# Optimization experiments

Hardware: AMD Instinct MI355X
Metric: run time of the kernel (lower is better)

Reference implementation:

```python
import jax, jax.numpy as jnp
import numpy as np

HEADS = 8
HEAD_DIM = 32
DIM = 256        # embed_dim; inner_dim = HEADS*HEAD_DIM = 256
DEPTH = 2
MLP_DIM = 1024
GRID_H, GRID_W = 64, 64
CELL_DIM = 15    # pe(0) + in(3) + out(3) + hidden(9)
PE_IN = 3        # cell_pe_patch_dim + cell_in_patch_dim
UPDATE_DIM = 12  # cell_out(3) + hidden(9)
BATCH = 8


def layer_norm(x, g, b, eps=1e-5):
    m = jnp.mean(x, axis=-1, keepdims=True)
    v = jnp.var(x, axis=-1, keepdims=True)
    return (x - m) * jax.lax.rsqrt(v + eps) * g + b


def vit_positional_encoding(n, dim):
    pos = jnp.arange(n, dtype=jnp.float32)[:, None]
    div = jnp.exp(jnp.arange(0, dim, 2, dtype=jnp.float32) * (-np.log(10000.0) / dim))
    pe = jnp.zeros((n, dim), dtype=jnp.float32)
    pe = pe.at[:, 0::2].set(jnp.sin(pos * div)).at[:, 1::2].set(jnp.cos(pos * div))
    return pe[None]  # [1, n, dim]


def localize(x, H, W):
    # x: [b, heads, n, d] with n = H*W. Gather circular 3x3 neighbourhood per position
    # (equivalent to circular pad + one-hot conv in the torch LocalizeAttention).
    b, nh, n, d = x.shape
    y = x.reshape(b, nh, H, W, d)
    neigh = [jnp.roll(y, (1 - ki, 1 - kj), axis=(2, 3)) for ki in range(3) for kj in range(3)]
    return jnp.stack(neigh, axis=4).reshape(b, nh, n, 9, d)  # [b, h, n, 9, d]


def setup_inputs() -> dict:
    key = jax.random.key(0)
    ks = jax.random.split(key, 20)
    d = {}
    d['cells'] = jax.random.normal(ks[0], (BATCH, CELL_DIM, GRID_H, GRID_W), dtype=jnp.float32)
    s = 0.02
    d['We'] = jax.random.normal(ks[1], (CELL_DIM, DIM), jnp.float32) * s
    d['be'] = jnp.zeros((DIM,), jnp.float32)
    d['ln1_g'] = jnp.ones((DEPTH, DIM), jnp.float32)
    d['ln1_b'] = jnp.zeros((DEPTH, DIM), jnp.float32)
    d['Wqkv'] = jax.random.normal(ks[2], (DEPTH, DIM, 3 * HEADS * HEAD_DIM), jnp.float32) * s
    d['Wo'] = jax.random.normal(ks[3], (DEPTH, HEADS * HEAD_DIM, DIM), jnp.float32) * s
    d['bo'] = jnp.zeros((DEPTH, DIM), jnp.float32)
    d['ln2_g'] = jnp.ones((DEPTH, DIM), jnp.float32)
    d['ln2_b'] = jnp.zeros((DEPTH, DIM), jnp.float32)
    d['W1'] = jax.random.normal(ks[4], (DEPTH, DIM, MLP_DIM), jnp.float32) * s
    d['b1'] = jnp.zeros((DEPTH, MLP_DIM), jnp.float32)
    d['W2'] = jax.random.normal(ks[5], (DEPTH, MLP_DIM, DIM), jnp.float32) * s
    d['b2'] = jnp.zeros((DEPTH, DIM), jnp.float32)
    d['lnh_g'] = jnp.ones((DIM,), jnp.float32)
    d['lnh_b'] = jnp.zeros((DIM,), jnp.float32)
    # NOTE: torch zero-inits mlp_head; we use small random weights so the output is nontrivial.
    d['Wh'] = jax.random.normal(ks[6], (DIM, UPDATE_DIM), jnp.float32) * s
    d['bh'] = jnp.zeros((UPDATE_DIM,), jnp.float32)
    return d


def reference(cells, We, be, ln1_g, ln1_b, Wqkv, Wo, bo, ln2_g, ln2_b,
              W1, b1, W2, b2, lnh_g, lnh_b, Wh, bh):
    b, c, H, W = cells.shape
    n = H * W
    x = cells.reshape(b, c, n).transpose(0, 2, 1)           # b n c
    x = x @ We + be                                         # cell_to_embedding
    x = x + vit_positional_encoding(n, x.shape[-1])
    scale = HEAD_DIM ** -0.5
    for l in range(DEPTH):
        y = layer_norm(x, ln1_g[l], ln1_b[l])
        qkv = y @ Wqkv[l]                                   # b n 3*inner
        q, k, v = jnp.split(qkv, 3, axis=-1)
        split_heads = lambda t: t.reshape(b, n, HEADS, HEAD_DIM).transpose(0, 2, 1, 3)
        q, k, v = split_heads(q), split_heads(k), split_heads(v)  # b h n d
        kl = localize(k, H, W)                              # b h n 9 d
        vl = localize(v, H, W)
        dots = jnp.einsum('bhnd,bhnkd->bhnk', q, kl) * scale
        attn = jax.nn.softmax(dots, axis=-1)
        out = jnp.einsum('bhnk,bhnkd->bhnd', attn, vl)
        out = out.transpose(0, 2, 1, 3).reshape(b, n, HEADS * HEAD_DIM)
        x = out @ Wo[l] + bo[l] + x                         # attention + residual
        y = layer_norm(x, ln2_g[l], ln2_b[l])
        y = jax.nn.gelu(y @ W1[l] + b1[l], approximate=False) @ W2[l] + b2[l]
        x = x + y                                           # ffn + residual
    upd = layer_norm(x, lnh_g, lnh_b) @ Wh + bh             # b n UPDATE_DIM
    upd = upd.transpose(0, 2, 1).reshape(b, UPDATE_DIM, H, W)
    # update_rate = 1.0 -> deterministic branch: cells[:, PE_IN:] + update
    updated = cells[:, PE_IN:] + upd
    return jnp.concatenate([cells[:, :PE_IN], updated], axis=1)
```

## Files before the change

### kernel.cpp

```cpp
#include <hip/hip_runtime.h>
#include <hip/hip_bf16.h>
#include <math.h>

#define HEADS 8
#define HEAD_DIM 32
#define DIM 256
#define MLP_DIM 1024
#define NTOK 4096
#define BATCH 8
#define M_TOK (BATCH*NTOK)
#define CELL_DIM 15
#define PE_IN 3
#define UPD 12
#define HME ((size_t)M_TOK*32)

typedef __attribute__((ext_vector_type(8))) short bf16x8;
typedef __attribute__((ext_vector_type(4))) float f32x4;

static __device__ __forceinline__ float bf2f(unsigned short u) {
    return __uint_as_float(((unsigned int)u) << 16);
}
static __device__ __forceinline__ unsigned short f2bf(float f) {
    __hip_bfloat16 h = __float2bfloat16(f);
    union { __hip_bfloat16 h; unsigned short u; } cv; cv.h = h; return cv.u;
}
static __device__ __forceinline__ void gload_lds16(const unsigned short* g, unsigned short* l) {
    __builtin_amdgcn_global_load_lds(
        (const __attribute__((address_space(1))) void*)g,
        (__attribute__((address_space(3))) void*)l, 16, 0, 0);
}
static __device__ __forceinline__ float gelu_fast(float v) {
    return v / (1.f + __expf(-1.59576912f * (v + 0.044715f * v * v * v)));
}

__global__ __launch_bounds__(256) void k_embed(const float* __restrict__ cells,
        const float* __restrict__ We, const float* __restrict__ be,
        const float* __restrict__ g, const float* __restrict__ bln,
        unsigned short* __restrict__ x, unsigned short* __restrict__ y) {
    __shared__ float red[8];
    int tok = blockIdx.x;
    int d = threadIdx.x;
    int b = tok >> 12, n = tok & 4095;
    const float* cb = cells + (size_t)b * CELL_DIM * NTOK + n;
    float acc = 0.f;
#pragma unroll
    for (int c = 0; c < CELL_DIM; ++c)
        acc += cb[c * NTOK] * We[c * DIM + d];
    int i = d >> 1;
    float freq = __expf(-0.03597789f * (float)(2 * i));
    float ph = (float)n * freq;
    float pe = (d & 1) ? __cosf(ph) : __sinf(ph);
    float v = acc + be[d] + pe;
    x[(size_t)tok * DIM + d] = f2bf(v);
    float s = v, ss = v * v;
#pragma unroll
    for (int off = 32; off; off >>= 1) { s += __shfl_xor(s, off); ss += __shfl_xor(ss, off); }
    int wave = d >> 6, lane = d & 63;
    if (lane == 0) { red[wave] = s; red[4 + wave] = ss; }
    __syncthreads();
    float stot = red[0] + red[1] + red[2] + red[3];
    float sstot = red[4] + red[5] + red[6] + red[7];
    float mean = stot * (1.f / DIM);
    float rstd = rsqrtf(sstot * (1.f / DIM) - mean * mean + 1e-5f);
    y[(size_t)tok * DIM + d] = f2bf((v - mean) * rstd * g[d] + bln[d]);
}

__global__ __launch_bounds__(256) void k_prep(const float* __restrict__ Wqkv,
        const float* __restrict__ Wo, const float* __restrict__ W1,
        const float* __restrict__ W2, const float* __restrict__ Wh,
        unsigned short* __restrict__ wT) {
    int seg = blockIdx.y;
    int idx = blockIdx.x * 256 + threadIdx.x;
    if (seg == 8) {
        if (idx >= 16 * 256) return;
        int u = idx >> 8, k = idx & 255;
        wT[1572864 + idx] = (u < UPD) ? f2bf(Wh[(size_t)k * UPD + u]) : (unsigned short)0;
        return;
    }
    int l = seg >> 2, mat = seg & 3;
    const float* src; int kwSh, Nw; size_t ooff;
    switch (mat) {
        case 0: src = Wqkv + (size_t)l * 196608; kwSh = 8;  Nw = 768;  ooff = (size_t)l * 786432 + 0;      break;
        case 1: src = Wo   + (size_t)l * 65536;  kwSh = 8;  Nw = 256;  ooff = (size_t)l * 786432 + 196608; break;
        case 2: src = W1   + (size_t)l * 262144; kwSh = 8;  Nw = 1024; ooff = (size_t)l * 786432 + 262144; break;
        default:src = W2   + (size_t)l * 262144; kwSh = 10; Nw = 256;  ooff = (size_t)l * 786432 + 524288; break;
    }
    int Kw = 1 << kwSh;
    if (idx >= Kw * Nw) return;
    int n = idx >> kwSh, k = idx & (Kw - 1);
    wT[ooff + idx] = f2bf(src[(size_t)k * Nw + n]);
}

template<int EPI, int KT>
__global__ __launch_bounds__(512, 4) void k_mgemm(const unsigned short* __restrict__ A,
        const unsigned short* __restrict__ BT, const float* __restrict__ bias,
        void* __restrict__ Cout, int M, int N, int NT) {
    __shared__ unsigned short As[3][128 * 32];
    __shared__ unsigned short Bs[3][256 * 32];
    int bid = blockIdx.x;
    int cpx = gridDim.x >> 3;
    int sb = (bid & 7) * cpx + (bid >> 3);
    int mt = sb / NT, nt = sb - mt * NT;
    int m0 = mt * 128, n0 = nt * 256;
    int t = threadIdx.x;
    int lane = t & 63, w = t >> 6;
    int wm = (w >> 2) * 64, wn = (w & 3) * 64;
    f32x4 acc[4][4] = {};
    int rA = t >> 2, cgA = (t & 3) ^ ((rA >> 1) & 3);
    const unsigned short* aBase = A + (size_t)(m0 + rA) * KT + cgA * 8;
    int rB0 = t >> 2, cgB0 = (t & 3) ^ ((rB0 >> 1) & 3);
    int c1 = t + 512;
    int rB1 = c1 >> 2, cgB1 = (c1 & 3) ^ ((rB1 >> 1) & 3);
    const unsigned short* b0Base = BT + (size_t)(n0 + rB0) * KT + cgB0 * 8;
    const unsigned short* b1Base = BT + (size_t)(n0 + rB1) * KT + cgB1 * 8;
    int fr = lane & 15, kb8 = lane >> 4;

    auto stage = [&](int buf, int k0) {
        gload_lds16(aBase + k0,  &As[0][0] + buf * 4096 + t * 8);
        gload_lds16(b0Base + k0, &Bs[0][0] + buf * 8192 + t * 8);
        gload_lds16(b1Base + k0, &Bs[0][0] + buf * 8192 + 4096 + t * 8);
    };
    auto compute = [&](int buf) {
        const unsigned short* a = &As[0][0] + buf * 4096;
        const unsigned short* b = &Bs[0][0] + buf * 8192;
        bf16x8 af[4], bfv[4];
#pragma unroll
        for (int i = 0; i < 4; ++i) {
            int r_ = wm + i * 16 + fr;
            af[i] = *(const bf16x8*)&a[r_ * 32 + ((kb8 ^ ((r_ >> 1) & 3)) << 3)];
        }
#pragma unroll
        for (int j = 0; j < 4; ++j) {
            int r_ = wn + j * 16 + fr;
            bfv[j] = *(const bf16x8*)&b[r_ * 32 + ((kb8 ^ ((r_ >> 1) & 3)) << 3)];
        }
        __builtin_amdgcn_s_setprio(1);
#pragma unroll
        for (int i = 0; i < 4; ++i)
#pragma unroll
            for (int j = 0; j < 4; ++j)
                acc[i][j] = __builtin_amdgcn_mfma_f32_16x16x32_bf16(bfv[j], af[i], acc[i][j], 0, 0, 0);
        __builtin_amdgcn_s_setprio(0);
    };

    constexpr int NK = KT >> 5;
    stage(0, 0);
    stage(1, 32);
    asm volatile("s_waitcnt vmcnt(3)" ::: "memory");
    __builtin_amdgcn_s_barrier();
    __builtin_amdgcn_sched_barrier(0);
#pragma unroll
    for (int k = 0; k < NK - 1; ++k) {
        if (k + 2 < NK) stage((k + 2) % 3, (k + 2) * 32);
        compute(k % 3);
        __builtin_amdgcn_sched_barrier(0);
        if (k + 2 < NK) asm volatile("s_waitcnt vmcnt(3)" ::: "memory");
        else            asm volatile("s_waitcnt vmcnt(0)" ::: "memory");
        __builtin_amdgcn_s_barrier();
        __builtin_amdgcn_sched_barrier(0);
    }
    compute((NK - 1) % 3);

    int mcol = lane & 15, nq = (lane >> 4) * 4;
#pragma unroll
    for (int i = 0; i < 4; ++i) {
        int m = m0 + wm + i * 16 + mcol;
#pragma unroll
        for (int j = 0; j < 4; ++j) {
            int ng = n0 + wn + j * 16 + nq;
            if (EPI == 3) {
                int type = ng >> 8, rem = ng & 255;
                ushort4 pk;
                pk.x = f2bf(acc[i][j][0]); pk.y = f2bf(acc[i][j][1]);
                pk.z = f2bf(acc[i][j][2]); pk.w = f2bf(acc[i][j][3]);
                *(ushort4*)((unsigned short*)Cout +
                    (size_t)(type * 8 + (rem >> 5)) * HME + (size_t)m * 32 + (rem & 31)) = pk;
            } else {
                float4 b4 = *(const float4*)&bias[ng];
                ushort4 pk;
                pk.x = f2bf(gelu_fast(acc[i][j][0] + b4.x));
                pk.y = f2bf(gelu_fast(acc[i][j][1] + b4.y));
                pk.z = f2bf(gelu_fast(acc[i][j][2] + b4.z));
                pk.w = f2bf(gelu_fast(acc[i][j][3] + b4.w));
                *(ushort4*)((unsigned short*)Cout + (size_t)m * N + ng) = pk;
            }
        }
    }
}

template<int ALAYOUT>
__global__ __launch_bounds__(512, 4) void k_mgemm_ln(const unsigned short* __restrict__ A,
        const unsigned short* __restrict__ BT, const float* __restrict__ bias,
        const float* __restrict__ g, const float* __restrict__ bln,
        unsigned short* __restrict__ x, unsigned short* __restrict__ y, int K) {
    __shared__ unsigned short As[3][64 * 32];
    __shared__ unsigned short Bs[3][256 * 32];
    float* sred = (float*)&As[0][0];
    float* ssred = sred + 512;
    float* msr = ssred + 512;
    int t = threadIdx.x;
    int lane = t & 63, w = t >> 6;
    int wn = w * 32;
    int m0 = blockIdx.x * 64;
    int mloc = lane & 15, nq = (lane >> 4) * 4;

    ushort4 xres[4][2];
#pragma unroll
    for (int i = 0; i < 4; ++i) {
        int gm = m0 + i * 16 + mloc;
#pragma unroll
        for (int j = 0; j < 2; ++j)
            xres[i][j] = *(const ushort4*)&x[(size_t)gm * DIM + wn + j * 16 + nq];
    }
    __builtin_amdgcn_sched_barrier(0);

    f32x4 acc[4][2] = {};
    int rB0 = t >> 2, cgB0 = (t & 3) ^ ((rB0 >> 1) & 3);
    int c1 = t + 512;
    int rB1 = c1 >> 2, cgB1 = (c1 & 3) ^ ((rB1 >> 1) & 3);
    int tA = t & 255;
    int rA = tA >> 2, cgA = (tA & 3) ^ ((rA >> 1) & 3);
    const unsigned short* aBase = (ALAYOUT == 0)
        ? A + (size_t)(m0 + rA) * K + cgA * 8
        : A + (size_t)(m0 + rA) * 32 + cgA * 8;
    const unsigned short* b0Base = BT + (size_t)rB0 * K + cgB0 * 8;
    const unsigned short* b1Base = BT + (size_t)rB1 * K + cgB1 * 8;
    int fr = lane & 15, kb8 = lane >> 4;

    auto stage = [&](int buf, int k0) {
        unsigned short* as_ = &As[0][0] + buf * 2048;
        unsigned short* bs_ = &Bs[0][0] + buf * 8192;
        gload_lds16(b0Base + k0, bs_ + t * 8);
        gload_lds16(b1Base + k0, bs_ + 4096 + t * 8);
        if (t < 256) {
            const unsigned short* aSrc = (ALAYOUT == 0) ? aBase + k0 : aBase + (size_t)(k0 >> 5) * HME;
            gload_lds16(aSrc, as_ + tA * 8);
        } else {
            gload_lds16(b0Base + k0, bs_ + t * 8);
        }
    };
    auto compute = [&](int buf) {
        const unsigned short* as_ = &As[0][0] + buf * 2048;
        const unsigned short* bs_ = &Bs[0][0] + buf * 8192;
        bf16x8 af[4], bfv[2];
#pragma unroll
        for (int i = 0; i < 4; ++i) {
            int r_ = i * 16 + fr;
            af[i] = *(const bf16x8*)&as_[r_ * 32 + ((kb8 ^ ((r_ >> 1) & 3)) << 3)];
        }
#pragma unroll
        for (int j = 0; j < 2; ++j) {
            int rl = wn + j * 16 + fr;
            bfv[j] = *(const bf16x8*)&bs_[rl * 32 + ((kb8 ^ ((rl >> 1) & 3)) << 3)];
        }
        __builtin_amdgcn_s_setprio(1);
#pragma unroll
        for (int i = 0; i < 4; ++i)
#pragma unroll
            for (int j = 0; j < 2; ++j)
                acc[i][j] = __builtin_amdgcn_mfma_f32_16x16x32_bf16(bfv[j], af[i], acc[i][j], 0, 0, 0);
        __builtin_amdgcn_s_setprio(0);
    };

    int nk = K >> 5;
    stage(0, 0);
    stage(1, 32);
    asm volatile("s_waitcnt vmcnt(3)" ::: "memory");
    __builtin_amdgcn_s_barrier();
    __builtin_amdgcn_sched_barrier(0);
    int cur = 0;
    for (int k = 0; k < nk - 1; ++k) {
        int pre = k + 2;
        if (pre < nk) {
            int preBuf = cur + 2; if (preBuf >= 3) preBuf -= 3;
            stage(preBuf, pre * 32);
        }
        compute(cur);
        __builtin_amdgcn_sched_barrier(0);
        if (pre < nk) asm volatile("s_waitcnt vmcnt(3)" ::: "memory");
        else          asm volatile("s_waitcnt vmcnt(0)" ::: "memory");
        __builtin_amdgcn_s_barrier();
        __builtin_amdgcn_sched_barrier(0);
        ++cur; if (cur >= 3) cur -= 3;
    }
    compute(cur);
    __syncthreads();

#pragma unroll
    for (int i = 0; i < 4; ++i) {
        float s = 0.f, ss = 0.f;
#pragma unroll
        for (int j = 0; j < 2; ++j) {
            int nb = wn + j * 16 + nq;
            float4 b4 = *(const float4*)&bias[nb];
            acc[i][j][0] += b4.x + bf2f(xres[i][j].x);
            acc[i][j][1] += b4.y + bf2f(xres[i][j].y);
            acc[i][j][2] += b4.z + bf2f(xres[i][j].z);
            acc[i][j][3] += b4.w + bf2f(xres[i][j].w);
#pragma unroll
            for (int r = 0; r < 4; ++r) { float v = acc[i][j][r]; s += v; ss += v * v; }
        }
        s += __shfl_xor(s, 16); ss += __shfl_xor(ss, 16);
        s += __shfl_xor(s, 32); ss += __shfl_xor(ss, 32);
        if (lane < 16) {
            int row = i * 16 + lane;
            sred[row * 8 + w] = s;
            ssred[row * 8 + w] = ss;
        }
    }
    __syncthreads();
    if (t < 64) {
        float s = 0.f, ss = 0.f;
#pragma unroll
        for (int q = 0; q < 8; ++q) { s += sred[t * 8 + q]; ss += ssred[t * 8 + q]; }
        float mean = s * (1.f / DIM);
        float var = ss * (1.f / DIM) - mean * mean;
        msr[t * 2] = mean;
        msr[t * 2 + 1] = rsqrtf(var + 1e-5f);
    }
    __syncthreads();
#pragma unroll
    for (int i = 0; i < 4; ++i) {
        int row = i * 16 + mloc;
        int gm = m0 + row;
        float mean = msr[row * 2], rstd = msr[row * 2 + 1];
#pragma unroll
        for (int j = 0; j < 2; ++j) {
            int nb = wn + j * 16 + nq;
            float4 gv4 = *(const float4*)&g[nb];
            float4 bb4 = *(const float4*)&bln[nb];
            ushort4 xo;
            xo.x = f2bf(acc[i][j][0]); xo.y = f2bf(acc[i][j][1]);
            xo.z = f2bf(acc[i][j][2]); xo.w = f2bf(acc[i][j][3]);
            *(ushort4*)&x[(size_t)gm * DIM + nb] = xo;
            ushort4 yv;
            yv.x = f2bf((acc[i][j][0] - mean) * rstd * gv4.x + bb4.x);
            yv.y = f2bf((acc[i][j][1] - mean) * rstd * gv4.y + bb4.y);
            yv.z = f2bf((acc[i][j][2] - mean) * rstd * gv4.z + bb4.z);
            yv.w = f2bf((acc[i][j][3] - mean) * rstd * gv4.w + bb4.w);
            *(ushort4*)&y[(size_t)gm * DIM + nb] = yv;
        }
    }
}

__global__ __launch_bounds__(256) void k_attn(const unsigned short* __restrict__ qkvH,
        unsigned short* __restrict__ attnH) {
    __shared__ unsigned short Ks[324 * 40];
    __shared__ unsigned short Vs[324 * 40];
    int bid = blockIdx.x;
    int b = bid >> 7, h = (bid >> 4) & 7, pr = (bid >> 2) & 3, pc = bid & 3;
    int t = threadIdx.x;
    int ty = t >> 4, tx = t & 15;
    const unsigned short* kplane = qkvH + (size_t)(8 + h) * HME;
    const unsigned short* vplane = qkvH + (size_t)(16 + h) * HME;

    int tok = (b << 12) + ((pr * 16 + ty) << 6) + (pc * 16 + tx);
    float q[32];
    {
        const uint4* u = (const uint4*)(qkvH + (size_t)h * HME + (size_t)tok * 32);
#pragma unroll
        for (int i = 0; i < 4; ++i) {
            uint4 x4 = u[i];
            unsigned wv[4] = {x4.x, x4.y, x4.z, x4.w};
#pragma unroll
            for (int wj = 0; wj < 4; ++wj) {
                q[i * 8 + wj * 2]     = __uint_as_float(wv[wj] << 16);
                q[i * 8 + wj * 2 + 1] = __uint_as_float(wv[wj] & 0xffff0000u);
            }
        }
    }
    for (int s = t; s < 324; s += 256) {
        int sr = s / 18, sc = s - sr * 18;
        int gr = (pr * 16 + sr - 1) & 63, gc = (pc * 16 + sc - 1) & 63;
        size_t nt = ((size_t)b << 12) + (gr << 6) + gc;
        const uint4* ksrc = (const uint4*)(kplane + nt * 32);
        const uint4* vsrc = (const uint4*)(vplane + nt * 32);
#pragma unroll
        for (int i = 0; i < 4; ++i) {
            *(uint4*)&Ks[s * 40 + i * 8] = ksrc[i];
            *(uint4*)&Vs[s * 40 + i * 8] = vsrc[i];
        }
    }
    __syncthreads();

    float dots[9];
    int slots[9];
#pragma unroll
    for (int ki = 0; ki < 3; ++ki)
#pragma unroll
        for (int kj = 0; kj < 3; ++kj) {
            int slot = (ty + ki) * 18 + (tx + kj);
            slots[ki * 3 + kj] = slot;
            const unsigned short* kp = &Ks[slot * 40];
            float acc = 0.f;
#pragma unroll
            for (int i = 0; i < 4; ++i) {
                uint4 x4 = *(const uint4*)(kp + i * 8);
                unsigned wv[4] = {x4.x, x4.y, x4.z, x4.w};
#pragma unroll
                for (int wj = 0; wj < 4; ++wj) {
                    acc += __uint_as_float(wv[wj] << 16)         * q[i * 8 + wj * 2];
                    acc += __uint_as_float(wv[wj] & 0xffff0000u) * q[i * 8 + wj * 2 + 1];
                }
            }
            dots[ki * 3 + kj] = acc * 0.17677669529f;
        }
    float m = dots[0];
#pragma unroll
    for (int j = 1; j < 9; ++j) m = fmaxf(m, dots[j]);
    float sum = 0.f;
#pragma unroll
    for (int j = 0; j < 9; ++j) { dots[j] = __expf(dots[j] - m); sum += dots[j]; }
    float inv = 1.f / sum;
    float o[32] = {};
#pragma unroll
    for (int j = 0; j < 9; ++j) {
        float wgt = dots[j] * inv;
        const unsigned short* vp = &Vs[slots[j] * 40];
#pragma unroll
        for (int i = 0; i < 4; ++i) {
            uint4 x4 = *(const uint4*)(vp + i * 8);
            unsigned wv[4] = {x4.x, x4.y, x4.z, x4.w};
#pragma unroll
            for (int wj = 0; wj < 4; ++wj) {
                o[i * 8 + wj * 2]     += wgt * __uint_as_float(wv[wj] << 16);
                o[i * 8 + wj * 2 + 1] += wgt * __uint_as_float(wv[wj] & 0xffff0000u);
            }
        }
    }
    uint4 st[4];
    unsigned* sw = (unsigned*)st;
#pragma unroll
    for (int i = 0; i < 16; ++i)
        sw[i] = (unsigned)f2bf(o[2 * i]) | ((unsigned)f2bf(o[2 * i + 1]) << 16);
    uint4* od = (uint4*)(attnH + (size_t)h * HME + (size_t)tok * 32);
#pragma unroll
    for (int i = 0; i < 4; ++i) od[i] = st[i];
}

__global__ __launch_bounds__(256) void k_headgemv(const unsigned short* __restrict__ y,
        const unsigned short* __restrict__ WhT, float* __restrict__ Cg) {
    int t = threadIdx.x, lane = t & 63, w = t >> 6;
    int m0 = blockIdx.x * 64 + w * 16;
    int fr = lane & 15, kb = (lane >> 4) * 8;
    f32x4 acc = {};
    const unsigned short* aRow = y + (size_t)(m0 + fr) * DIM + kb;
    const unsigned short* bRow = WhT + (size_t)fr * DIM + kb;
#pragma unroll
    for (int k0 = 0; k0 < DIM; k0 += 32) {
        bf16x8 a = *(const bf16x8*)(aRow + k0);
        bf16x8 bfr = *(const bf16x8*)(bRow + k0);
        acc = __builtin_amdgcn_mfma_f32_16x16x32_bf16(a, bfr, acc, 0, 0, 0);
    }
    int col = lane & 15, rowq = (lane >> 4) * 4;
#pragma unroll
    for (int r = 0; r < 4; ++r)
        Cg[(size_t)(m0 + rowq + r) * 16 + col] = acc[r];
}

__global__ __launch_bounds__(256) void k_assemble(const float* __restrict__ cells,
        const float* __restrict__ Cg, const float* __restrict__ bh,
        float* __restrict__ outp) {
    int idx = blockIdx.x * 256 + threadIdx.x;
    int total = BATCH * CELL_DIM * (NTOK / 4);
    if (idx >= total) return;
    int n4 = idx & 1023;
    int c = (idx >> 10) % CELL_DIM;
    int b = idx / (CELL_DIM * 1024);
    size_t ci = ((size_t)b * CELL_DIM + c) * NTOK + n4 * 4;
    float4 o = *(const float4*)(cells + ci);
    if (c >= PE_IN) {
        int u = c - PE_IN;
        float bias = bh[u];
        size_t tok = (size_t)b * NTOK + n4 * 4;
        o.x += Cg[(tok + 0) * 16 + u] + bias;
        o.y += Cg[(tok + 1) * 16 + u] + bias;
        o.z += Cg[(tok + 2) * 16 + u] + bias;
        o.w += Cg[(tok + 3) * 16 + u] + bias;
    }
    *(float4*)(outp + ci) = o;
}

extern "C" void kernel_launch(void* const* d_in, const int* in_sizes, int n_in,
                              void* d_out, int out_size, void* d_ws, size_t ws_size,
                              hipStream_t stream) {
    const float* cells = (const float*)d_in[0];
    const float* We    = (const float*)d_in[1];
    const float* be    = (const float*)d_in[2];
    const float* ln1_g = (const float*)d_in[3];
    const float* ln1_b = (const float*)d_in[4];
    const float* Wqkv  = (const float*)d_in[5];
    const float* Wo    = (const float*)d_in[6];
    const float* bo    = (const float*)d_in[7];
    const float* ln2_g = (const float*)d_in[8];
    const float* ln2_b = (const float*)d_in[9];
    const float* W1    = (const float*)d_in[10];
    const float* b1    = (const float*)d_in[11];
    const float* W2    = (const float*)d_in[12];
    const float* b2    = (const float*)d_in[13];
    const float* lnh_g = (const float*)d_in[14];
    const float* lnh_b = (const float*)d_in[15];
    const float* Wh    = (const float*)d_in[16];
    const float* bh    = (const float*)d_in[17];
    float* outp = (float*)d_out;

    char* ws = (char*)d_ws;
    unsigned short* x = (unsigned short*)ws;
    unsigned short* y = (unsigned short*)(ws + 33554432);
    unsigned short* scratch = (unsigned short*)(ws + 50331648);
    unsigned short* wT = (unsigned short*)(ws + 117440512);
    unsigned short* qkvH  = scratch;
    unsigned short* attnH = scratch + 24 * HME;
    unsigned short* hidden = scratch;
    float* Cg = (float*)scratch;

    k_prep<<<dim3(1024, 9), 256, 0, stream>>>(Wqkv, Wo, W1, W2, Wh, wT);
    k_embed<<<M_TOK, 256, 0, stream>>>(cells, We, be, ln1_g, ln1_b, x, y);
    for (int l = 0; l < 2; ++l) {
        const unsigned short* wL = wT + (size_t)l * 786432;
        const float* gN = (l == 0) ? ln1_g + DIM : lnh_g;
        const float* bN = (l == 0) ? ln1_b + DIM : lnh_b;
        k_mgemm<3, 256><<<768, 512, 0, stream>>>(
            y, wL + 0, nullptr, qkvH, M_TOK, 768, 3);
        k_attn<<<1024, 256, 0, stream>>>(qkvH, attnH);
        k_mgemm_ln<1><<<M_TOK / 64, 512, 0, stream>>>(
            attnH, wL + 196608, bo + l * DIM, ln2_g + l * DIM, ln2_b + l * DIM, x, y, DIM);
        k_mgemm<1, 256><<<1024, 512, 0, stream>>>(
            y, wL + 262144, b1 + l * MLP_DIM, hidden, M_TOK, MLP_DIM, 4);
        k_mgemm_ln<0><<<M_TOK / 64, 512, 0, stream>>>(
            hidden, wL + 524288, b2 + l * DIM, gN, bN, x, y, MLP_DIM);
    }
    k_headgemv<<<M_TOK / 64, 256, 0, stream>>>(y, wT + 1572864, Cg);
    k_assemble<<<(BATCH * CELL_DIM * (NTOK / 4) + 255) / 256, 256, 0, stream>>>(cells, Cg, bh, outp);
}
```

Baseline: 323.5 us.

## Enlarge fused GEMM+LayerNorm tile to 128 rows with 2x4 warp grid

The GEMM+LayerNorm kernel now processes 128 rows per block instead of 64. Its 8 waves are arranged as a 2x4 grid, each computing a 64x64 sub-tile, so every staged weight tile is reused across twice as many rows and global B traffic is halved. The residual x is loaded in the epilogue rather than prefetched before the main loop. This costs more accumulator registers and LDS per block, and the grid shrinks to 256 blocks, which may limit occupancy and parallelism.

```diff
diff --git a/kernel.cpp b/kernel.cpp
--- a/kernel.cpp
+++ b/kernel.cpp
@@ -193,71 +193,54 @@
         const unsigned short* __restrict__ BT, const float* __restrict__ bias,
         const float* __restrict__ g, const float* __restrict__ bln,
         unsigned short* __restrict__ x, unsigned short* __restrict__ y, int K) {
-    __shared__ unsigned short As[3][64 * 32];
+    __shared__ unsigned short As[3][128 * 32];
     __shared__ unsigned short Bs[3][256 * 32];
     float* sred = (float*)&As[0][0];
     float* ssred = sred + 512;
     float* msr = ssred + 512;
     int t = threadIdx.x;
     int lane = t & 63, w = t >> 6;
-    int wn = w * 32;
-    int m0 = blockIdx.x * 64;
-    int mloc = lane & 15, nq = (lane >> 4) * 4;
-
-    ushort4 xres[4][2];
-#pragma unroll
-    for (int i = 0; i < 4; ++i) {
-        int gm = m0 + i * 16 + mloc;
-#pragma unroll
-        for (int j = 0; j < 2; ++j)
-            xres[i][j] = *(const ushort4*)&x[(size_t)gm * DIM + wn + j * 16 + nq];
-    }
-    __builtin_amdgcn_sched_barrier(0);
-
-    f32x4 acc[4][2] = {};
+    int wm = (w >> 2) * 64, wn = (w & 3) * 64, wq = w & 3;
+    int m0 = blockIdx.x * 128;
+    int mcol = lane & 15, nq = (lane >> 4) * 4;
+
+    f32x4 acc[4][4] = {};
+    int rA = t >> 2, cgA = (t & 3) ^ ((rA >> 1) & 3);
+    const unsigned short* aBase = (ALAYOUT == 0)
+        ? A + (size_t)(m0 + rA) * K + cgA * 8
+        : A + (size_t)(m0 + rA) * 32 + cgA * 8;
     int rB0 = t >> 2, cgB0 = (t & 3) ^ ((rB0 >> 1) & 3);
     int c1 = t + 512;
     int rB1 = c1 >> 2, cgB1 = (c1 & 3) ^ ((rB1 >> 1) & 3);
-    int tA = t & 255;
-    int rA = tA >> 2, cgA = (tA & 3) ^ ((rA >> 1) & 3);
-    const unsigned short* aBase = (ALAYOUT == 0)
-        ? A + (size_t)(m0 + rA) * K + cgA * 8
-        : A + (size_t)(m0 + rA) * 32 + cgA * 8;
     const unsigned short* b0Base = BT + (size_t)rB0 * K + cgB0 * 8;
     const unsigned short* b1Base = BT + (size_t)rB1 * K + cgB1 * 8;
     int fr = lane & 15, kb8 = lane >> 4;
 
     auto stage = [&](int buf, int k0) {
-        unsigned short* as_ = &As[0][0] + buf * 2048;
-        unsigned short* bs_ = &Bs[0][0] + buf * 8192;
-        gload_lds16(b0Base + k0, bs_ + t * 8);
-        gload_lds16(b1Base + k0, bs_ + 4096 + t * 8);
-        if (t < 256) {
-            const unsigned short* aSrc = (ALAYOUT == 0) ? aBase + k0 : aBase + (size_t)(k0 >> 5) * HME;
-            gload_lds16(aSrc, as_ + tA * 8);
-        } else {
-            gload_lds16(b0Base + k0, bs_ + t * 8);
-        }
+        const unsigned short* aSrc = (ALAYOUT == 0) ? aBase + k0 : aBase + (size_t)(k0 >> 5) * HME;
+        gload_lds16(aSrc,        &As[0][0] + buf * 4096 + t * 8);
+        gload_lds16(b0Base + k0, &Bs[0][0] + buf * 8192 + t * 8);
+        gload_lds16(b1Base + k0, &Bs[0][0] + buf * 8192 + 4096 + t * 8);
     };
     auto compute = [&](int buf) {
-        const unsigned short* as_ = &As[0][0] + buf * 2048;
-        const unsigned short* bs_ = &Bs[0][0] + buf * 8192;
-        bf16x8 af[4], bfv[2];
+        const unsigned short* a = &As[0][0] + buf * 4096;
+        const unsigned short* b = &Bs[0][0] + buf * 8192;
+        bf16x8 af[4], bfv[4];
 #pragma unroll
         for (int i = 0; i < 4; ++i) {
-            int r_ = i * 16 + fr;
-            af[i] = *(const bf16x8*)&as_[r_ * 32 + ((kb8 ^ ((r_ >> 1) & 3)) << 3)];
-        }
-#pragma unroll
-        for (int j = 0; j < 2; ++j) {
-            int rl = wn + j * 16 + fr;
-            bfv[j] = *(const bf16x8*)&bs_[rl * 32 + ((kb8 ^ ((rl >> 1) & 3)) << 3)];
+            int r_ = wm + i * 16 + fr;
+            af[i] = *(const bf16x8*)&a[r_ * 32 + ((kb8 ^ ((r_ >> 1) & 3)) << 3)];
+        }
+#pragma unroll
+        for (int j = 0; j < 4; ++j) {
+            int r_ = wn + j * 16 + fr;
+            bfv[j] = *(const bf16x8*)&b[r_ * 32 + ((kb8 ^ ((r_ >> 1) & 3)) << 3)];
         }
         __builtin_amdgcn_s_setprio(1);
 #pragma unroll
         for (int i = 0; i < 4; ++i)
 #pragma unroll
-            for (int j = 0; j < 2; ++j)
+            for (int j = 0; j < 4; ++j)
                 acc[i][j] = __builtin_amdgcn_mfma_f32_16x16x32_bf16(bfv[j], af[i], acc[i][j], 0, 0, 0);
         __builtin_amdgcn_s_setprio(0);
     };
@@ -288,31 +271,32 @@
 
 #pragma unroll
     for (int i = 0; i < 4; ++i) {
+        int gm = m0 + wm + i * 16 + mcol;
         float s = 0.f, ss = 0.f;
 #pragma unroll
-        for (int j = 0; j < 2; ++j) {
+        for (int j = 0; j < 4; ++j) {
             int nb = wn + j * 16 + nq;
+            ushort4 xr = *(const ushort4*)&x[(size_t)gm * DIM + nb];
             float4 b4 = *(const float4*)&bias[nb];
-            acc[i][j][0] += b4.x + bf2f(xres[i][j].x);
-            acc[i][j][1] += b4.y + bf2f(xres[i][j].y);
-            acc[i][j][2] += b4.z + bf2f(xres[i][j].z);
-            acc[i][j][3] += b4.w + bf2f(xres[i][j].w);
+            acc[i][j][0] += b4.x + bf2f(xr.x);
+            acc[i][j][1] += b4.y + bf2f(xr.y);
+            acc[i][j][2] += b4.z + bf2f(xr.z);
+            acc[i][j][3] += b4.w + bf2f(xr.w);
 #pragma unroll
             for (int r = 0; r < 4; ++r) { float v = acc[i][j][r]; s += v; ss += v * v; }
         }
         s += __shfl_xor(s, 16); ss += __shfl_xor(ss, 16);
         s += __shfl_xor(s, 32); ss += __shfl_xor(ss, 32);
         if (lane < 16) {
-            int row = i * 16 + lane;
-            sred[row * 8 + w] = s;
-            ssred[row * 8 + w] = ss;
+            int row = wm + i * 16 + lane;
+            sred[row * 4 + wq] = s;
+            ssred[row * 4 + wq] = ss;
         }
     }
     __syncthreads();
-    if (t < 64) {
-        float s = 0.f, ss = 0.f;
-#pragma unroll
-        for (int q = 0; q < 8; ++q) { s += sred[t * 8 + q]; ss += ssred[t * 8 + q]; }
+    if (t < 128) {
+        float s = sred[t * 4] + sred[t * 4 + 1] + sred[t * 4 + 2] + sred[t * 4 + 3];
+        float ss = ssred[t * 4] + ssred[t * 4 + 1] + ssred[t * 4 + 2] + ssred[t * 4 + 3];
         float mean = s * (1.f / DIM);
         float var = ss * (1.f / DIM) - mean * mean;
         msr[t * 2] = mean;
@@ -321,11 +305,11 @@
     __syncthreads();
 #pragma unroll
     for (int i = 0; i < 4; ++i) {
-        int row = i * 16 + mloc;
+        int row = wm + i * 16 + mcol;
         int gm = m0 + row;
         float mean = msr[row * 2], rstd = msr[row * 2 + 1];
 #pragma unroll
-        for (int j = 0; j < 2; ++j) {
+        for (int j = 0; j < 4; ++j) {
             int nb = wn + j * 16 + nq;
             float4 gv4 = *(const float4*)&g[nb];
             float4 bb4 = *(const float4*)&bln[nb];
@@ -523,11 +507,11 @@
         k_mgemm<3, 256><<<768, 512, 0, stream>>>(
             y, wL + 0, nullptr, qkvH, M_TOK, 768, 3);
         k_attn<<<1024, 256, 0, stream>>>(qkvH, attnH);
-        k_mgemm_ln<1><<<M_TOK / 64, 512, 0, stream>>>(
+        k_mgemm_ln<1><<<M_TOK / 128, 512, 0, stream>>>(
             attnH, wL + 196608, bo + l * DIM, ln2_g + l * DIM, ln2_b + l * DIM, x, y, DIM);
         k_mgemm<1, 256><<<1024, 512, 0, stream>>>(
             y, wL + 262144, b1 + l * MLP_DIM, hidden, M_TOK, MLP_DIM, 4);
-        k_mgemm_ln<0><<<M_TOK / 64, 512, 0, stream>>>(
+        k_mgemm_ln<0><<<M_TOK / 128, 512, 0, stream>>>(
             hidden, wL + 524288, b2 + l * DIM, gN, bN, x, y, MLP_DIM);
     }
     k_headgemv<<<M_TOK / 64, 256, 0, stream>>>(y, wT + 1572864, Cg);
```

Result: slower. 331.5 us (+2.5%).
